# Kernel tuning notes

Measured on AMD Instinct MI355X. Metric: run time of the kernel, lower is better.

Reference implementation:

```python
import jax, jax.numpy as jnp
import numpy as np

N_NODES = 20000
N_EDGES = 320000
N_GRAPHS = 64


def gat_conv(x, src, dst, W, a_src, a_dst, bias, heads, ch, concat):
    # x: [N, F_in]; W: [F_in, heads*ch]; a_src/a_dst: [heads, ch]
    N = x.shape[0]
    h = (x @ W).reshape(N, heads, ch)                       # [N, H, C]
    alpha_s = jnp.sum(h * a_src, axis=-1)                   # [N, H]
    alpha_d = jnp.sum(h * a_dst, axis=-1)                   # [N, H]
    e = jax.nn.leaky_relu(alpha_s[src] + alpha_d[dst], 0.2) # [E, H]
    # segment softmax over incoming edges of each destination node
    m = jax.ops.segment_max(e, dst, num_segments=N)         # [N, H]
    ex = jnp.exp(e - m[dst])
    denom = jax.ops.segment_sum(ex, dst, num_segments=N)    # [N, H]
    alpha = ex / (denom[dst] + 1e-16)                       # [E, H]
    msg = h[src] * alpha[:, :, None]                        # [E, H, C]
    out = jax.ops.segment_sum(msg, dst, num_segments=N)     # [N, H, C]
    out = out.reshape(N, heads * ch) if concat else out.mean(axis=1)
    return out + bias, alpha


def setup_inputs() -> dict:
    key = jax.random.key(0)
    ks = jax.random.split(key, 24)
    dim_in, md, dim_out = 8, 64, 128
    hid = md * 4  # 256
    p = lambda k, shape: jax.random.normal(k, shape, dtype=jnp.float32) * 0.1
    inp = {
        "x_ppi": jax.random.normal(ks[0], (N_NODES, dim_in), dtype=jnp.float32),
        "ppi_edge_index": jax.random.randint(ks[1], (2, N_EDGES), 0, N_NODES),
        "ppi_batch": jnp.sort(jax.random.randint(ks[2], (N_NODES,), 0, N_GRAPHS)),
        # GATConv 1: dim_in -> 64, heads=4, concat
        "W1": p(ks[3], (dim_in, 4 * md)), "a_src1": p(ks[4], (4, md)), "a_dst1": p(ks[5], (4, md)), "b_gat1": jnp.zeros((hid,), jnp.float32),
        "lw1": p(ks[6], (dim_in, hid)), "lb1": jnp.zeros((hid,), jnp.float32),
        # GATConv 2: 256 -> 64, heads=4, concat
        "W2": p(ks[7], (hid, 4 * md)), "a_src2": p(ks[8], (4, md)), "a_dst2": p(ks[9], (4, md)), "b_gat2": jnp.zeros((hid,), jnp.float32),
        "lw2": p(ks[10], (hid, hid)), "lb2": jnp.zeros((hid,), jnp.float32),
        # GATConv 3: 256 -> 128, heads=6, concat=False (mean)
        "W3": p(ks[11], (hid, 6 * dim_out)), "a_src3": p(ks[12], (6, dim_out)), "a_dst3": p(ks[13], (6, dim_out)), "b_gat3": jnp.zeros((dim_out,), jnp.float32),
        "lw3": p(ks[14], (hid, dim_out)), "lb3": jnp.zeros((dim_out,), jnp.float32),
        # BatchNorm1d(dim_out), training-mode batch statistics
        "bn_gamma": jnp.ones((dim_out,), jnp.float32), "bn_beta": jnp.zeros((dim_out,), jnp.float32),
    }
    return inp


def reference(x_ppi, ppi_edge_index, ppi_batch,
              W1, a_src1, a_dst1, b_gat1, lw1, lb1,
              W2, a_src2, a_dst2, b_gat2, lw2, lb2,
              W3, a_src3, a_dst3, b_gat3, lw3, lb3,
              bn_gamma, bn_beta):
    src, dst = ppi_edge_index[0], ppi_edge_index[1]
    g1, _ = gat_conv(x_ppi, src, dst, W1, a_src1, a_dst1, b_gat1, heads=4, ch=64, concat=True)
    x = jax.nn.relu(g1 + x_ppi @ lw1 + lb1)
    g2, _ = gat_conv(x, src, dst, W2, a_src2, a_dst2, b_gat2, heads=4, ch=64, concat=True)
    x = jax.nn.relu(g2 + x @ lw2 + lb2)
    x_res = x @ lw3 + lb3
    g3, att = gat_conv(x, src, dst, W3, a_src3, a_dst3, b_gat3, heads=6, ch=128, concat=False)
    x = g3 + x_res
    x = jax.nn.relu(x)
    # BatchNorm1d, training mode (biased variance, eps=1e-5)
    mu = x.mean(axis=0)
    var = jnp.mean((x - mu) ** 2, axis=0)
    x = (x - mu) * jax.lax.rsqrt(var + 1e-5) * bn_gamma + bn_beta
    # global max pool over graphs
    pooled = jax.ops.segment_max(x, ppi_batch, num_segments=N_GRAPHS)
    return pooled, att
```

## Files before the change

kernel.cpp:

```cpp
#include <hip/hip_runtime.h>
#include <hip/hip_bf16.h>
#include <math.h>

#define N_NODES 20000
#define N_EDGES 320000
#define N_GRAPHS 64

typedef __bf16 bf16_t;
typedef bf16_t bf16x8 __attribute__((ext_vector_type(8)));
typedef bf16_t bf16x4 __attribute__((ext_vector_type(4)));
typedef bf16_t bf16x2 __attribute__((ext_vector_type(2)));
typedef float f32x4 __attribute__((ext_vector_type(4)));
typedef float f32x2 __attribute__((ext_vector_type(2)));

__global__ void hist_k(const int* __restrict__ dst, int* __restrict__ deg, int E) {
    int e = blockIdx.x * 256 + threadIdx.x;
    if (e < E) atomicAdd(&deg[dst[e]], 1);
}

__global__ __launch_bounds__(1024) void scan_k(const int* __restrict__ deg,
                                               int* __restrict__ offs,
                                               int* __restrict__ cursor, int n) {
    __shared__ int s_ws[16];
    int tid = threadIdx.x;
    int lane = tid & 63, w = tid >> 6;
    int carry = 0;
    for (int base = 0; base < n; base += 1024) {
        int i = base + tid;
        int v = (i < n) ? deg[i] : 0;
        int x = v;
        #pragma unroll
        for (int off = 1; off < 64; off <<= 1) {
            int t = __shfl_up(x, off);
            if (lane >= off) x += t;
        }
        if (lane == 63) s_ws[w] = x;
        __syncthreads();
        if (tid < 16) {
            int y = s_ws[tid];
            #pragma unroll
            for (int off = 1; off < 16; off <<= 1) {
                int t = __shfl_up(y, off);
                if (tid >= off) y += t;
            }
            s_ws[tid] = y;
        }
        __syncthreads();
        int wbase = (w > 0) ? s_ws[w - 1] : 0;
        int ex = carry + wbase + x - v;
        if (i < n) { offs[i] = ex; cursor[i] = ex; }
        carry += s_ws[15];
        __syncthreads();
    }
    if (tid == 0) offs[n] = carry;
}

__global__ void scatter_k(const int* __restrict__ src, const int* __restrict__ dst,
                          int* __restrict__ cursor, int* __restrict__ csr_src,
                          int* __restrict__ csr_eid, int E) {
    int e = blockIdx.x * 256 + threadIdx.x;
    if (e < E) {
        int d = dst[e];
        int p = atomicAdd(&cursor[d], 1);
        csr_src[p] = src[e];
        csr_eid[p] = e;
    }
}

__global__ __launch_bounds__(256) void wt_k(const float* __restrict__ W,
                                            bf16_t* __restrict__ Bt, int K, int N) {
    __shared__ float t[32][33];
    int k0 = blockIdx.y * 32, n0 = blockIdx.x * 32;
    int tx = threadIdx.x & 31, ty = threadIdx.x >> 5;
    for (int i = ty; i < 32; i += 8) t[i][tx] = W[(size_t)(k0 + i) * N + n0 + tx];
    __syncthreads();
    for (int i = ty; i < 32; i += 8)
        Bt[(size_t)(n0 + i) * K + k0 + tx] = (bf16_t)t[tx][i];
}

template <typename OUT>
__global__ __launch_bounds__(256) void gemm_k(const float* __restrict__ A,
                                              const float* __restrict__ B,
                                              OUT* __restrict__ C,
                                              const float* __restrict__ bias,
                                              int M, int N, int K,
                                              const float* __restrict__ asv,
                                              const float* __restrict__ adv,
                                              float* __restrict__ as_o,
                                              float* __restrict__ ad_o,
                                              int H, int Ch) {
    __shared__ float As[16][65];
    __shared__ float Bs[16][64];
    int tid = threadIdx.x;
    int tx = tid & 15, ty = tid >> 4;
    int row0 = blockIdx.y * 64, col0 = blockIdx.x * 64;
    float acc[4][4] = {};
    for (int k0 = 0; k0 < K; k0 += 16) {
        #pragma unroll
        for (int i = 0; i < 4; ++i) {
            int idx = tid + i * 256;
            int m = idx >> 4, kk = idx & 15;
            int gm = row0 + m, gk = k0 + kk;
            As[kk][m] = (gm < M && gk < K) ? A[(size_t)gm * K + gk] : 0.f;
        }
        #pragma unroll
        for (int i = 0; i < 4; ++i) {
            int idx = tid + i * 256;
            int kk = idx >> 6, n = idx & 63;
            int gk = k0 + kk, gn = col0 + n;
            Bs[kk][n] = (gk < K && gn < N) ? B[(size_t)gk * N + gn] : 0.f;
        }
        __syncthreads();
        #pragma unroll
        for (int kk = 0; kk < 16; ++kk) {
            float a[4], b[4];
            #pragma unroll
            for (int i = 0; i < 4; ++i) a[i] = As[kk][ty * 4 + i];
            #pragma unroll
            for (int j = 0; j < 4; ++j) b[j] = Bs[kk][tx * 4 + j];
            #pragma unroll
            for (int i = 0; i < 4; ++i)
                #pragma unroll
                for (int j = 0; j < 4; ++j) acc[i][j] += a[i] * b[j];
        }
        __syncthreads();
    }
    #pragma unroll
    for (int i = 0; i < 4; ++i) {
        int gm = row0 + ty * 4 + i;
        if (gm >= M) continue;
        #pragma unroll
        for (int j = 0; j < 4; ++j) {
            int gn = col0 + tx * 4 + j;
            if (gn < N) C[(size_t)gm * N + gn] = (OUT)(acc[i][j] + (bias ? bias[gn] : 0.f));
        }
    }
    if (asv) {
        int hd = col0 / Ch;
        float av[4], dv[4];
        #pragma unroll
        for (int j = 0; j < 4; ++j) {
            int ca = col0 + tx * 4 + j;
            av[j] = asv[ca];
            dv[j] = adv[ca];
        }
        #pragma unroll
        for (int i = 0; i < 4; ++i) {
            float sp = 0.f, sd = 0.f;
            #pragma unroll
            for (int j = 0; j < 4; ++j) { sp += acc[i][j] * av[j]; sd += acc[i][j] * dv[j]; }
            #pragma unroll
            for (int m = 1; m < 16; m <<= 1) {
                sp += __shfl_xor(sp, m);
                sd += __shfl_xor(sd, m);
            }
            if (tx == 0) {
                int gm = row0 + ty * 4 + i;
                if (gm < M) { as_o[gm * H + hd] = sp; ad_o[gm * H + hd] = sd; }
            }
        }
    }
}

template <typename OUT>
__global__ __launch_bounds__(256) void gemm_bf16_k(
    const bf16_t* __restrict__ A, const bf16_t* __restrict__ Bt,
    OUT* __restrict__ C, const float* __restrict__ bias, int M, int N, int K,
    const float* __restrict__ asv, const float* __restrict__ adv,
    float* __restrict__ as_o, float* __restrict__ ad_o, int H, int Ch) {
    __shared__ bf16_t As[128][40];
    __shared__ bf16_t Bs[128][40];
    int tid = threadIdx.x;
    int row0 = blockIdx.y * 128, col0 = blockIdx.x * 128;
    int wave = tid >> 6, lane = tid & 63, quad = lane >> 4, l16 = lane & 15;
    int wm = wave >> 1, wn = wave & 1;
    f32x4 acc[4][4] = {};
    int sr = tid >> 2;
    int sc = (tid & 3) * 8;
    for (int k0 = 0; k0 < K; k0 += 32) {
        #pragma unroll
        for (int half = 0; half < 2; ++half) {
            int r = sr + half * 64;
            int gm = row0 + r;
            bf16x8 v = {};
            if (gm < M) v = *(const bf16x8*)&A[(size_t)gm * K + k0 + sc];
            *(bf16x8*)&As[r][sc] = v;
            int gn = col0 + r;
            bf16x8 w = {};
            if (gn < N) w = *(const bf16x8*)&Bt[(size_t)gn * K + k0 + sc];
            *(bf16x8*)&Bs[r][sc] = w;
        }
        __syncthreads();
        bf16x8 af[4], bfr[4];
        #pragma unroll
        for (int i = 0; i < 4; ++i) {
            af[i] = *(const bf16x8*)&As[wm * 64 + i * 16 + l16][quad * 8];
            bfr[i] = *(const bf16x8*)&Bs[wn * 64 + i * 16 + l16][quad * 8];
        }
        #pragma unroll
        for (int i = 0; i < 4; ++i)
            #pragma unroll
            for (int j = 0; j < 4; ++j)
                acc[i][j] = __builtin_amdgcn_mfma_f32_16x16x32_bf16(af[i], bfr[j],
                                                                   acc[i][j], 0, 0, 0);
        __syncthreads();
    }
    #pragma unroll
    for (int i = 0; i < 4; ++i) {
        int base_m = row0 + wm * 64 + i * 16 + quad * 4;
        #pragma unroll
        for (int j = 0; j < 4; ++j) {
            int gn = col0 + wn * 64 + j * 16 + l16;
            float bv = bias ? bias[gn] : 0.f;
            #pragma unroll
            for (int r = 0; r < 4; ++r) {
                int gm = base_m + r;
                if (gm < M) C[(size_t)gm * N + gn] = (OUT)(acc[i][j][r] + bv);
            }
        }
    }
    if (asv) {
        int hd = (col0 + wn * 64) / Ch;
        float av[4], dv[4];
        #pragma unroll
        for (int j = 0; j < 4; ++j) {
            int ca = col0 + wn * 64 + j * 16 + l16;
            av[j] = asv[ca];
            dv[j] = adv[ca];
        }
        #pragma unroll
        for (int i = 0; i < 4; ++i) {
            float sp[4] = {}, sd[4] = {};
            #pragma unroll
            for (int j = 0; j < 4; ++j)
                #pragma unroll
                for (int r = 0; r < 4; ++r) {
                    sp[r] += acc[i][j][r] * av[j];
                    sd[r] += acc[i][j][r] * dv[j];
                }
            #pragma unroll
            for (int m = 1; m < 16; m <<= 1)
                #pragma unroll
                for (int r = 0; r < 4; ++r) {
                    sp[r] += __shfl_xor(sp[r], m);
                    sd[r] += __shfl_xor(sd[r], m);
                }
            if (l16 == 0) {
                #pragma unroll
                for (int r = 0; r < 4; ++r) {
                    int gm = row0 + wm * 64 + i * 16 + quad * 4 + r;
                    if (gm < M) {
                        if (Ch == 128) {
                            atomicAdd(&as_o[gm * H + hd], sp[r]);
                            atomicAdd(&ad_o[gm * H + hd], sd[r]);
                        } else {
                            as_o[gm * H + hd] = sp[r];
                            ad_o[gm * H + hd] = sd[r];
                        }
                    }
                }
            }
        }
    }
}

__device__ __forceinline__ float leaky02(float v) { return v > 0.f ? v : 0.2f * v; }

__global__ __launch_bounds__(256) void agg_concat_k(
    const bf16_t* __restrict__ h, const float* __restrict__ as_,
    const float* __restrict__ ad_, const int* __restrict__ offs,
    const int* __restrict__ csr_src, const float* __restrict__ lin,
    const float* __restrict__ bgat, bf16_t* __restrict__ xb) {
    int j = blockIdx.x;
    int tid = threadIdx.x;
    int o0 = offs[j], deg = offs[j + 1] - o0;
    __shared__ int s_src[64];
    __shared__ float s_adj[4];
    __shared__ float s_ws[8][4];
    __shared__ float s_inv[4];
    __shared__ float s_red[8][256];
    if (tid < 4) s_adj[tid] = ad_[j * 4 + tid];
    int g = tid >> 5;
    int u = tid & 31;
    int myh = u >> 3;
    const char* hbase = (const char*)h + u * 16;
    f32x4 acc0 = {}, acc1 = {};
    float wsum = 0.f;
    for (int e0 = 0; e0 < deg; e0 += 64) {
        int ne = min(64, deg - e0);
        if (tid < ne) s_src[tid] = csr_src[o0 + e0 + tid];
        __syncthreads();
        float adj = s_adj[myh];
        #pragma unroll 2
        for (int e = g; e < ne; e += 8) {
            int s = s_src[e];
            float w = __expf(leaky02(as_[s * 4 + myh] + adj));
            bf16x8 v = *(const bf16x8*)(hbase + s * 512);
            wsum += w;
            #pragma unroll
            for (int i = 0; i < 4; ++i) acc0[i] += w * (float)v[i];
            #pragma unroll
            for (int i = 0; i < 4; ++i) acc1[i] += w * (float)v[4 + i];
        }
        __syncthreads();
    }
    if ((u & 7) == 0) s_ws[g][myh] = wsum;
    *(f32x4*)&s_red[g][u * 8] = acc0;
    *(f32x4*)&s_red[g][u * 8 + 4] = acc1;
    __syncthreads();
    if (tid < 4) {
        float d = 0.f;
        #pragma unroll
        for (int g2 = 0; g2 < 8; ++g2) d += s_ws[g2][tid];
        s_inv[tid] = 1.f / (d + 1e-16f);
    }
    __syncthreads();
    {
        int c = tid;
        float s = 0.f;
        #pragma unroll
        for (int g2 = 0; g2 < 8; ++g2) s += s_red[g2][c];
        float v = fmaxf(s * s_inv[c >> 6] + bgat[c] + lin[(size_t)j * 256 + c], 0.f);
        xb[(size_t)j * 256 + c] = (bf16_t)v;
    }
}

__global__ __launch_bounds__(256) void agg_mean_k(
    const bf16_t* __restrict__ h, const float* __restrict__ as_,
    const float* __restrict__ ad_, const int* __restrict__ offs,
    const int* __restrict__ csr_src, const int* __restrict__ csr_eid,
    const float* __restrict__ xres, const float* __restrict__ bgat,
    float* __restrict__ y, float* __restrict__ att) {
    int j = blockIdx.x;
    int tid = threadIdx.x;
    int o0 = offs[j], deg = offs[j + 1] - o0;
    __shared__ int s_src[64];
    __shared__ float s_adj[6];
    __shared__ float s_ws[2][6];
    __shared__ float s_inv[6];
    __shared__ float s_red[2][768];
    if (tid < 6) s_adj[tid] = ad_[j * 6 + tid];
    int g = tid / 96;
    int u = tid - g * 96;
    int myh = u >> 4;
    const char* hbase = (const char*)h + u * 16;
    f32x4 acc0 = {}, acc1 = {};
    float wsum = 0.f;
    for (int e0 = 0; e0 < deg; e0 += 64) {
        int ne = min(64, deg - e0);
        if (tid < ne) s_src[tid] = csr_src[o0 + e0 + tid];
        __syncthreads();
        if (tid < 192) {
            float adj = s_adj[myh];
            #pragma unroll 4
            for (int e = g; e < ne; e += 2) {
                int s = s_src[e];
                float w = __expf(leaky02(as_[s * 6 + myh] + adj));
                bf16x8 v = *(const bf16x8*)(hbase + s * 1536);
                wsum += w;
                #pragma unroll
                for (int i = 0; i < 4; ++i) acc0[i] += w * (float)v[i];
                #pragma unroll
                for (int i = 0; i < 4; ++i) acc1[i] += w * (float)v[4 + i];
            }
        }
        __syncthreads();
    }
    if (tid < 192) {
        if ((u & 15) == 0) s_ws[g][myh] = wsum;
        *(f32x4*)&s_red[g][u * 8] = acc0;
        *(f32x4*)&s_red[g][u * 8 + 4] = acc1;
    }
    __syncthreads();
    if (tid < 6) {
        float d = s_ws[0][tid] + s_ws[1][tid];
        s_inv[tid] = 1.f / (d + 1e-16f);
    }
    __syncthreads();
    if (tid < 128) {
        float s = 0.f;
        #pragma unroll
        for (int hh = 0; hh < 6; ++hh)
            s += (s_red[0][hh * 128 + tid] + s_red[1][hh * 128 + tid]) * s_inv[hh];
        y[(size_t)j * 128 + tid] =
            fmaxf(s * (1.f / 6.f) + bgat[tid] + xres[(size_t)j * 128 + tid], 0.f);
    } else if (tid >= 192) {
        int t = tid - 192;
        for (int e = t; e < deg; e += 64) {
            int p = o0 + e;
            int s = csr_src[p];
            size_t eid = (size_t)csr_eid[p];
            #pragma unroll
            for (int hh = 0; hh < 6; ++hh) {
                float w = __expf(leaky02(as_[s * 6 + hh] + s_adj[hh])) * s_inv[hh];
                att[eid * 6 + hh] = w;
            }
        }
    }
}

__global__ void bn_stats_k(const float* __restrict__ y, float* __restrict__ sums, int N) {
    int c = threadIdx.x;
    float s = 0.f, q = 0.f;
    for (int r = blockIdx.x; r < N; r += gridDim.x) {
        float v = y[(size_t)r * 128 + c];
        s += v;
        q += v * v;
    }
    atomicAdd(&sums[c], s);
    atomicAdd(&sums[128 + c], q);
}
__global__ void bn_scale_k(const float* __restrict__ sums, const float* __restrict__ gamma,
                           const float* __restrict__ beta, float* __restrict__ scale,
                           float* __restrict__ shift, int N) {
    int c = threadIdx.x;
    float mu = sums[c] / (float)N;
    float var = fmaxf(sums[128 + c] / (float)N - mu * mu, 0.f);
    float inv = rsqrtf(var + 1e-5f) * gamma[c];
    scale[c] = inv;
    shift[c] = beta[c] - mu * inv;
}

__device__ __forceinline__ unsigned f2key(float f) {
    unsigned b = __float_as_uint(f);
    return (b & 0x80000000u) ? ~b : (b | 0x80000000u);
}
__global__ void pool_init_k(unsigned* __restrict__ pool_u) {
    int i = blockIdx.x * 256 + threadIdx.x;
    if (i < N_GRAPHS * 128) pool_u[i] = f2key(-3.402823466e38f * 2.0f);
}
__global__ void norm_pool_k(const float* __restrict__ y, const float* __restrict__ scale,
                            const float* __restrict__ shift, const int* __restrict__ batch,
                            unsigned* __restrict__ pool_u, int N) {
    int idx = blockIdx.x * 256 + threadIdx.x;
    if (idx >= N * 128) return;
    int n = idx >> 7, c = idx & 127;
    float v = y[idx] * scale[c] + shift[c];
    atomicMax(&pool_u[batch[n] * 128 + c], f2key(v));
}
__global__ void pool_write_k(const unsigned* __restrict__ pool_u, float* __restrict__ out) {
    int i = blockIdx.x * 256 + threadIdx.x;
    if (i < N_GRAPHS * 128) {
        unsigned u = pool_u[i];
        unsigned b = (u & 0x80000000u) ? (u & 0x7FFFFFFFu) : ~u;
        out[i] = __uint_as_float(b);
    }
}

extern "C" void kernel_launch(void* const* d_in, const int* in_sizes, int n_in,
                              void* d_out, int out_size, void* d_ws, size_t ws_size,
                              hipStream_t stream) {
    const int N = N_NODES, E = N_EDGES;
    const float* x_ppi = (const float*)d_in[0];
    const int* edge = (const int*)d_in[1];
    const int* batch = (const int*)d_in[2];
    const float* W1 = (const float*)d_in[3];
    const float* a_src1 = (const float*)d_in[4];
    const float* a_dst1 = (const float*)d_in[5];
    const float* b_gat1 = (const float*)d_in[6];
    const float* lw1 = (const float*)d_in[7];
    const float* lb1 = (const float*)d_in[8];
    const float* W2 = (const float*)d_in[9];
    const float* a_src2 = (const float*)d_in[10];
    const float* a_dst2 = (const float*)d_in[11];
    const float* b_gat2 = (const float*)d_in[12];
    const float* lw2 = (const float*)d_in[13];
    const float* lb2 = (const float*)d_in[14];
    const float* W3 = (const float*)d_in[15];
    const float* a_src3 = (const float*)d_in[16];
    const float* a_dst3 = (const float*)d_in[17];
    const float* b_gat3 = (const float*)d_in[18];
    const float* lw3 = (const float*)d_in[19];
    const float* lb3 = (const float*)d_in[20];
    const float* bn_gamma = (const float*)d_in[21];
    const float* bn_beta = (const float*)d_in[22];

    const int* src = edge;
    const int* dst = edge + E;

    size_t off = 0;
    auto alloc = [&](size_t bytes) {
        size_t o = off;
        off = (off + bytes + 255) & ~(size_t)255;
        return o;
    };
    char* ws = (char*)d_ws;
    bf16_t* xb = (bf16_t*)(ws + alloc((size_t)N * 256 * 2));
    bf16_t* hb = (bf16_t*)(ws + alloc((size_t)N * 768 * 2));
    float* lin = (float*)(ws + alloc((size_t)N * 256 * 4));
    float* x_res = (float*)(ws + alloc((size_t)N * 128 * 4));
    float* as_ = (float*)(ws + alloc((size_t)N * 6 * 4));
    float* ad_ = (float*)(ws + alloc((size_t)N * 6 * 4));
    int* deg = (int*)(ws + alloc((size_t)(N + 1) * 4));
    int* offs = (int*)(ws + alloc((size_t)(N + 1) * 4));
    int* cursor = (int*)(ws + alloc((size_t)(N + 1) * 4));
    int* csr_src = (int*)(ws + alloc((size_t)E * 4));
    int* csr_eid = (int*)(ws + alloc((size_t)E * 4));
    bf16_t* Wt2 = (bf16_t*)(ws + alloc((size_t)256 * 256 * 2));
    bf16_t* lwt2 = (bf16_t*)(ws + alloc((size_t)256 * 256 * 2));
    bf16_t* Wt3 = (bf16_t*)(ws + alloc((size_t)768 * 256 * 2));
    bf16_t* lwt3 = (bf16_t*)(ws + alloc((size_t)128 * 256 * 2));
    float* bn_sums = (float*)(ws + alloc(256 * 4));
    float* bn_scale = (float*)(ws + alloc(128 * 4));
    float* bn_shift = (float*)(ws + alloc(128 * 4));
    unsigned* pool_u = (unsigned*)(ws + alloc((size_t)N_GRAPHS * 128 * 4));

    float* out_pool = (float*)d_out;
    float* out_att = (float*)d_out + N_GRAPHS * 128;

    hipMemsetAsync(deg, 0, (size_t)N * 4, stream);
    hist_k<<<(E + 255) / 256, 256, 0, stream>>>(dst, deg, E);
    scan_k<<<1, 1024, 0, stream>>>(deg, offs, cursor, N);
    scatter_k<<<(E + 255) / 256, 256, 0, stream>>>(src, dst, cursor, csr_src, csr_eid, E);
    wt_k<<<dim3(8, 8), 256, 0, stream>>>(W2, Wt2, 256, 256);
    wt_k<<<dim3(8, 8), 256, 0, stream>>>(lw2, lwt2, 256, 256);
    wt_k<<<dim3(24, 8), 256, 0, stream>>>(W3, Wt3, 256, 768);
    wt_k<<<dim3(4, 8), 256, 0, stream>>>(lw3, lwt3, 256, 128);

    gemm_k<bf16_t><<<dim3(4, 313), 256, 0, stream>>>(x_ppi, W1, hb, nullptr, N, 256, 8,
                                                     a_src1, a_dst1, as_, ad_, 4, 64);
    gemm_k<float><<<dim3(4, 313), 256, 0, stream>>>(x_ppi, lw1, lin, lb1, N, 256, 8,
                                                    nullptr, nullptr, nullptr, nullptr, 0, 1);
    agg_concat_k<<<N, 256, 0, stream>>>(hb, as_, ad_, offs, csr_src, lin, b_gat1, xb);

    gemm_bf16_k<bf16_t><<<dim3(2, 157), 256, 0, stream>>>(xb, Wt2, hb, nullptr, N, 256, 256,
                                                          a_src2, a_dst2, as_, ad_, 4, 64);
    gemm_bf16_k<float><<<dim3(2, 157), 256, 0, stream>>>(xb, lwt2, lin, lb2, N, 256, 256,
                                                         nullptr, nullptr, nullptr, nullptr,
                                                         0, 1);
    agg_concat_k<<<N, 256, 0, stream>>>(hb, as_, ad_, offs, csr_src, lin, b_gat2, xb);

    hipMemsetAsync(as_, 0, (size_t)N * 6 * 4, stream);
    hipMemsetAsync(ad_, 0, (size_t)N * 6 * 4, stream);
    gemm_bf16_k<bf16_t><<<dim3(6, 157), 256, 0, stream>>>(xb, Wt3, hb, nullptr, N, 768, 256,
                                                          a_src3, a_dst3, as_, ad_, 6, 128);
    gemm_bf16_k<float><<<dim3(1, 157), 256, 0, stream>>>(xb, lwt3, x_res, lb3, N, 128, 256,
                                                         nullptr, nullptr, nullptr, nullptr,
                                                         0, 1);
    float* y = lin;
    agg_mean_k<<<N, 256, 0, stream>>>(hb, as_, ad_, offs, csr_src, csr_eid, x_res, b_gat3,
                                      y, out_att);

    hipMemsetAsync(bn_sums, 0, 256 * 4, stream);
    bn_stats_k<<<160, 128, 0, stream>>>(y, bn_sums, N);
    bn_scale_k<<<1, 128, 0, stream>>>(bn_sums, bn_gamma, bn_beta, bn_scale, bn_shift, N);

    pool_init_k<<<(N_GRAPHS * 128 + 255) / 256, 256, 0, stream>>>(pool_u);
    norm_pool_k<<<((size_t)N * 128 + 255) / 256, 256, 0, stream>>>(y, bn_scale, bn_shift, batch,
                                                                   pool_u, N);
    pool_write_k<<<(N_GRAPHS * 128 + 255) / 256, 256, 0, stream>>>(pool_u, out_pool);
}
```

Measured before the change: 525.6 us.

## Aggregate before projecting in GAT layers 1 and 3 using linearity

Layers 1 and 3 now aggregate the input features before the projection instead of projecting then aggregating. The attention logits come from precomputed W·a vectors, and the mean over heads, the residual linear and the biases are folded into one stacked GEMM (K=40 for layer 1, K=1792 for layer 3). This removes the large 768-wide hidden tensor and its per-edge gathers in layer 3, which now gather 256-wide rows. In exchange layer 3 writes a 1792-wide per-node buffer and runs a longer-K GEMM, and bf16 rounding moves to different points in the computation.

```diff
diff --git a/kernel.cpp b/kernel.cpp
--- a/kernel.cpp
+++ b/kernel.cpp
@@ -78,17 +78,69 @@
         Bt[(size_t)(n0 + i) * K + k0 + tx] = (bf16_t)t[tx][i];
 }
 
+__global__ void w3s_k(const float* __restrict__ W3, const float* __restrict__ lw3,
+                      bf16_t* __restrict__ Bt) {
+    int id = blockIdx.x * 256 + threadIdx.x;
+    if (id >= 128 * 1792) return;
+    int n = id / 1792, k = id - n * 1792;
+    float v;
+    if (k < 1536) {
+        int h = k >> 8, c = k & 255;
+        v = W3[(size_t)c * 768 + h * 128 + n] * (1.f / 6.f);
+    } else {
+        int c = k - 1536;
+        v = lw3[(size_t)c * 128 + n];
+    }
+    Bt[id] = (bf16_t)v;
+}
+
+__global__ void b40_k(const float* __restrict__ W1, const float* __restrict__ lw1,
+                      float* __restrict__ B) {
+    int id = blockIdx.x * 256 + threadIdx.x;
+    if (id >= 40 * 256) return;
+    int k = id >> 8, n = id & 255;
+    float v;
+    if (k < 32) {
+        int h = k >> 3, c = k & 7;
+        v = ((n >> 6) == h) ? W1[(size_t)c * 256 + n] : 0.f;
+    } else {
+        int c = k - 32;
+        v = lw1[(size_t)c * 256 + n];
+    }
+    B[id] = v;
+}
+
+__global__ void va_k(const float* __restrict__ W, const float* __restrict__ a_s,
+                     const float* __restrict__ a_d, float* __restrict__ Va,
+                     float* __restrict__ Vd, int H, int C) {
+    int k = blockIdx.x;
+    int lane = threadIdx.x;
+    const float* wr = W + (size_t)k * H * C;
+    for (int h = 0; h < H; ++h) {
+        float sa = 0.f, sd = 0.f;
+        for (int c = lane; c < C; c += 64) {
+            float wv = wr[h * C + c];
+            sa += wv * a_s[h * C + c];
+            sd += wv * a_d[h * C + c];
+        }
+        #pragma unroll
+        for (int m = 32; m; m >>= 1) { sa += __shfl_xor(sa, m); sd += __shfl_xor(sd, m); }
+        if (lane == 0) { Va[k * H + h] = sa; Vd[k * H + h] = sd; }
+    }
+}
+
+__global__ void addb_k(const float* __restrict__ a, const float* __restrict__ b,
+                       float* __restrict__ o, int n) {
+    int i = blockIdx.x * 256 + threadIdx.x;
+    if (i < n) o[i] = a[i] + b[i];
+}
+
 template <typename OUT>
 __global__ __launch_bounds__(256) void gemm_k(const float* __restrict__ A,
                                               const float* __restrict__ B,
                                               OUT* __restrict__ C,
                                               const float* __restrict__ bias,
-                                              int M, int N, int K,
-                                              const float* __restrict__ asv,
-                                              const float* __restrict__ adv,
-                                              float* __restrict__ as_o,
-                                              float* __restrict__ ad_o,
-                                              int H, int Ch) {
+                                              int M, int N, int K, int relu) {
     __shared__ float As[16][65];
     __shared__ float Bs[16][64];
     int tid = threadIdx.x;
@@ -132,31 +184,10 @@
         #pragma unroll
         for (int j = 0; j < 4; ++j) {
             int gn = col0 + tx * 4 + j;
-            if (gn < N) C[(size_t)gm * N + gn] = (OUT)(acc[i][j] + (bias ? bias[gn] : 0.f));
-        }
-    }
-    if (asv) {
-        int hd = col0 / Ch;
-        float av[4], dv[4];
-        #pragma unroll
-        for (int j = 0; j < 4; ++j) {
-            int ca = col0 + tx * 4 + j;
-            av[j] = asv[ca];
-            dv[j] = adv[ca];
-        }
-        #pragma unroll
-        for (int i = 0; i < 4; ++i) {
-            float sp = 0.f, sd = 0.f;
-            #pragma unroll
-            for (int j = 0; j < 4; ++j) { sp += acc[i][j] * av[j]; sd += acc[i][j] * dv[j]; }
-            #pragma unroll
-            for (int m = 1; m < 16; m <<= 1) {
-                sp += __shfl_xor(sp, m);
-                sd += __shfl_xor(sd, m);
-            }
-            if (tx == 0) {
-                int gm = row0 + ty * 4 + i;
-                if (gm < M) { as_o[gm * H + hd] = sp; ad_o[gm * H + hd] = sd; }
+            if (gn < N) {
+                float r = acc[i][j] + (bias ? bias[gn] : 0.f);
+                if (relu) r = fmaxf(r, 0.f);
+                C[(size_t)gm * N + gn] = (OUT)r;
             }
         }
     }
@@ -167,7 +198,7 @@
     const bf16_t* __restrict__ A, const bf16_t* __restrict__ Bt,
     OUT* __restrict__ C, const float* __restrict__ bias, int M, int N, int K,
     const float* __restrict__ asv, const float* __restrict__ adv,
-    float* __restrict__ as_o, float* __restrict__ ad_o, int H, int Ch) {
+    float* __restrict__ as_o, float* __restrict__ ad_o, int H, int Ch, int relu) {
     __shared__ bf16_t As[128][40];
     __shared__ bf16_t Bs[128][40];
     int tid = threadIdx.x;
@@ -215,7 +246,11 @@
             #pragma unroll
             for (int r = 0; r < 4; ++r) {
                 int gm = base_m + r;
-                if (gm < M) C[(size_t)gm * N + gn] = (OUT)(acc[i][j][r] + bv);
+                if (gm < M) {
+                    float rr = acc[i][j][r] + bv;
+                    if (relu) rr = fmaxf(rr, 0.f);
+                    C[(size_t)gm * N + gn] = (OUT)rr;
+                }
             }
         }
     }
@@ -250,13 +285,8 @@
                 for (int r = 0; r < 4; ++r) {
                     int gm = row0 + wm * 64 + i * 16 + quad * 4 + r;
                     if (gm < M) {
-                        if (Ch == 128) {
-                            atomicAdd(&as_o[gm * H + hd], sp[r]);
-                            atomicAdd(&ad_o[gm * H + hd], sd[r]);
-                        } else {
-                            as_o[gm * H + hd] = sp[r];
-                            ad_o[gm * H + hd] = sd[r];
-                        }
+                        as_o[gm * H + hd] = sp[r];
+                        ad_o[gm * H + hd] = sd[r];
                     }
                 }
             }
@@ -265,6 +295,90 @@
 }
 
 __device__ __forceinline__ float leaky02(float v) { return v > 0.f ? v : 0.2f * v; }
+
+__global__ void asad1_k(const float* __restrict__ x, const float* __restrict__ Va,
+                        const float* __restrict__ Vd, float* __restrict__ as_,
+                        float* __restrict__ ad_, int N) {
+    int idx = blockIdx.x * 256 + threadIdx.x;
+    if (idx >= N * 4) return;
+    int j = idx >> 2, h = idx & 3;
+    const float* xr = x + (size_t)j * 8;
+    float sa = 0.f, sd = 0.f;
+    #pragma unroll
+    for (int c = 0; c < 8; ++c) {
+        sa += xr[c] * Va[c * 4 + h];
+        sd += xr[c] * Vd[c * 4 + h];
+    }
+    as_[idx] = sa;
+    ad_[idx] = sd;
+}
+
+__global__ void asad3_k(const bf16_t* __restrict__ xb, const float* __restrict__ Va,
+                        const float* __restrict__ Vd, float* __restrict__ as_,
+                        float* __restrict__ ad_) {
+    int j = blockIdx.x;
+    int lane = threadIdx.x;
+    bf16x4 v = *(const bf16x4*)&xb[(size_t)j * 256 + lane * 4];
+    float sa[6] = {}, sd[6] = {};
+    #pragma unroll
+    for (int i = 0; i < 4; ++i) {
+        int k = lane * 4 + i;
+        float xv = (float)v[i];
+        #pragma unroll
+        for (int h = 0; h < 6; ++h) {
+            sa[h] += xv * Va[k * 6 + h];
+            sd[h] += xv * Vd[k * 6 + h];
+        }
+    }
+    #pragma unroll
+    for (int h = 0; h < 6; ++h) {
+        float a = sa[h], d = sd[h];
+        #pragma unroll
+        for (int m = 32; m; m >>= 1) { a += __shfl_xor(a, m); d += __shfl_xor(d, m); }
+        if (lane == 0) { as_[j * 6 + h] = a; ad_[j * 6 + h] = d; }
+    }
+}
+
+__global__ __launch_bounds__(256) void agg_z1_k(
+    const float* __restrict__ x, const float* __restrict__ as_,
+    const float* __restrict__ ad_, const int* __restrict__ offs,
+    const int* __restrict__ csr_src, float* __restrict__ z1) {
+    int j = blockIdx.x * 4 + (threadIdx.x >> 6);
+    int t = threadIdx.x & 63;
+    int e_l = t >> 3, c = t & 7;
+    int o0 = offs[j], deg = offs[j + 1] - o0;
+    float adj0 = ad_[j * 4 + 0], adj1 = ad_[j * 4 + 1];
+    float adj2 = ad_[j * 4 + 2], adj3 = ad_[j * 4 + 3];
+    float acc[4] = {}, ws[4] = {};
+    for (int e0 = 0; e0 < deg; e0 += 8) {
+        int ne = min(8, deg - e0);
+        if (e_l < ne) {
+            int s = csr_src[o0 + e0 + e_l];
+            float xv = x[(size_t)s * 8 + c];
+            f32x4 a = *(const f32x4*)&as_[s * 4];
+            float w0 = __expf(leaky02(a[0] + adj0));
+            float w1 = __expf(leaky02(a[1] + adj1));
+            float w2 = __expf(leaky02(a[2] + adj2));
+            float w3 = __expf(leaky02(a[3] + adj3));
+            acc[0] += w0 * xv; acc[1] += w1 * xv;
+            acc[2] += w2 * xv; acc[3] += w3 * xv;
+            ws[0] += w0; ws[1] += w1; ws[2] += w2; ws[3] += w3;
+        }
+    }
+    #pragma unroll
+    for (int m = 8; m < 64; m <<= 1)
+        #pragma unroll
+        for (int h = 0; h < 4; ++h) {
+            acc[h] += __shfl_xor(acc[h], m);
+            ws[h] += __shfl_xor(ws[h], m);
+        }
+    if (e_l == 0) {
+        #pragma unroll
+        for (int h = 0; h < 4; ++h)
+            z1[(size_t)j * 40 + h * 8 + c] = acc[h] / (ws[h] + 1e-16f);
+        z1[(size_t)j * 40 + 32 + c] = x[(size_t)j * 8 + c];
+    }
+}
 
 __global__ __launch_bounds__(256) void agg_concat_k(
     const bf16_t* __restrict__ h, const float* __restrict__ as_,
@@ -295,7 +409,7 @@
         for (int e = g; e < ne; e += 8) {
             int s = s_src[e];
             float w = __expf(leaky02(as_[s * 4 + myh] + adj));
-            bf16x8 v = *(const bf16x8*)(hbase + s * 512);
+            bf16x8 v = *(const bf16x8*)(hbase + (size_t)s * 512);
             wsum += w;
             #pragma unroll
             for (int i = 0; i < 4; ++i) acc0[i] += w * (float)v[i];
@@ -325,77 +439,86 @@
     }
 }
 
-__global__ __launch_bounds__(256) void agg_mean_k(
-    const bf16_t* __restrict__ h, const float* __restrict__ as_,
+__global__ __launch_bounds__(256) void agg_z3_k(
+    const bf16_t* __restrict__ xb, const float* __restrict__ as_,
     const float* __restrict__ ad_, const int* __restrict__ offs,
     const int* __restrict__ csr_src, const int* __restrict__ csr_eid,
-    const float* __restrict__ xres, const float* __restrict__ bgat,
-    float* __restrict__ y, float* __restrict__ att) {
+    bf16_t* __restrict__ z, float* __restrict__ att) {
     int j = blockIdx.x;
     int tid = threadIdx.x;
     int o0 = offs[j], deg = offs[j + 1] - o0;
+    __shared__ float s_adj[6], s_denom[6], s_inv[6];
     __shared__ int s_src[64];
-    __shared__ float s_adj[6];
-    __shared__ float s_ws[2][6];
-    __shared__ float s_inv[6];
-    __shared__ float s_red[2][768];
-    if (tid < 6) s_adj[tid] = ad_[j * 6 + tid];
-    int g = tid / 96;
-    int u = tid - g * 96;
-    int myh = u >> 4;
-    const char* hbase = (const char*)h + u * 16;
-    f32x4 acc0 = {}, acc1 = {};
-    float wsum = 0.f;
+    __shared__ float s_w[64 * 6];
+    __shared__ float s_red[8][6][256];
+    if (tid < 6) { s_adj[tid] = ad_[j * 6 + tid]; s_denom[tid] = 0.f; }
+    __syncthreads();
+    int g = tid >> 5;
+    int c = tid & 31;
+    const char* xbase = (const char*)xb + c * 16;
+    f32x4 a0[6] = {}, a1[6] = {};
     for (int e0 = 0; e0 < deg; e0 += 64) {
         int ne = min(64, deg - e0);
-        if (tid < ne) s_src[tid] = csr_src[o0 + e0 + tid];
-        __syncthreads();
-        if (tid < 192) {
-            float adj = s_adj[myh];
-            #pragma unroll 4
-            for (int e = g; e < ne; e += 2) {
-                int s = s_src[e];
-                float w = __expf(leaky02(as_[s * 6 + myh] + adj));
-                bf16x8 v = *(const bf16x8*)(hbase + s * 1536);
-                wsum += w;
+        #pragma unroll
+        for (int base = 0; base < 2; ++base) {
+            int idx = tid + base * 256;
+            if (idx < ne * 6) {
+                int e = idx / 6, h = idx - e * 6;
+                int s = csr_src[o0 + e0 + e];
+                if (h == 0) s_src[e] = s;
+                s_w[idx] = __expf(leaky02(as_[s * 6 + h] + s_adj[h]));
+            }
+        }
+        __syncthreads();
+        if (tid < 6) {
+            float d = 0.f;
+            for (int e = 0; e < ne; ++e) d += s_w[e * 6 + tid];
+            s_denom[tid] += d;
+        }
+        for (int e = g; e < ne; e += 8) {
+            int s = s_src[e];
+            bf16x8 v = *(const bf16x8*)(xbase + (size_t)s * 512);
+            float f0[4], f1[4];
+            #pragma unroll
+            for (int i = 0; i < 4; ++i) { f0[i] = (float)v[i]; f1[i] = (float)v[4 + i]; }
+            #pragma unroll
+            for (int h = 0; h < 6; ++h) {
+                float w = s_w[e * 6 + h];
                 #pragma unroll
-                for (int i = 0; i < 4; ++i) acc0[i] += w * (float)v[i];
-                #pragma unroll
-                for (int i = 0; i < 4; ++i) acc1[i] += w * (float)v[4 + i];
+                for (int i = 0; i < 4; ++i) {
+                    a0[h][i] += w * f0[i];
+                    a1[h][i] += w * f1[i];
+                }
             }
         }
         __syncthreads();
     }
-    if (tid < 192) {
-        if ((u & 15) == 0) s_ws[g][myh] = wsum;
-        *(f32x4*)&s_red[g][u * 8] = acc0;
-        *(f32x4*)&s_red[g][u * 8 + 4] = acc1;
-    }
+    #pragma unroll
+    for (int h = 0; h < 6; ++h) {
+        *(f32x4*)&s_red[g][h][c * 8] = a0[h];
+        *(f32x4*)&s_red[g][h][c * 8 + 4] = a1[h];
+    }
+    if (tid < 6) s_inv[tid] = 1.f / (s_denom[tid] + 1e-16f);
     __syncthreads();
-    if (tid < 6) {
-        float d = s_ws[0][tid] + s_ws[1][tid];
-        s_inv[tid] = 1.f / (d + 1e-16f);
-    }
-    __syncthreads();
-    if (tid < 128) {
-        float s = 0.f;
-        #pragma unroll
-        for (int hh = 0; hh < 6; ++hh)
-            s += (s_red[0][hh * 128 + tid] + s_red[1][hh * 128 + tid]) * s_inv[hh];
-        y[(size_t)j * 128 + tid] =
-            fmaxf(s * (1.f / 6.f) + bgat[tid] + xres[(size_t)j * 128 + tid], 0.f);
-    } else if (tid >= 192) {
-        int t = tid - 192;
-        for (int e = t; e < deg; e += 64) {
-            int p = o0 + e;
-            int s = csr_src[p];
-            size_t eid = (size_t)csr_eid[p];
-            #pragma unroll
-            for (int hh = 0; hh < 6; ++hh) {
-                float w = __expf(leaky02(as_[s * 6 + hh] + s_adj[hh])) * s_inv[hh];
-                att[eid * 6 + hh] = w;
-            }
-        }
+    {
+        int cc = tid;
+        #pragma unroll
+        for (int h = 0; h < 6; ++h) {
+            float s = 0.f;
+            #pragma unroll
+            for (int g2 = 0; g2 < 8; ++g2) s += s_red[g2][h][cc];
+            z[(size_t)j * 1792 + h * 256 + cc] = (bf16_t)(s * s_inv[h]);
+        }
+    }
+    if (tid < 32)
+        *(bf16x8*)&z[(size_t)j * 1792 + 1536 + tid * 8] =
+            *(const bf16x8*)&xb[(size_t)j * 256 + tid * 8];
+    for (int idx = tid; idx < deg * 6; idx += 256) {
+        int e = idx / 6, h = idx - e * 6;
+        int p = o0 + e;
+        int s = csr_src[p];
+        att[(size_t)csr_eid[p] * 6 + h] =
+            __expf(leaky02(as_[s * 6 + h] + s_adj[h])) * s_inv[h];
     }
 }
 
@@ -486,9 +609,11 @@
     };
     char* ws = (char*)d_ws;
     bf16_t* xb = (bf16_t*)(ws + alloc((size_t)N * 256 * 2));
-    bf16_t* hb = (bf16_t*)(ws + alloc((size_t)N * 768 * 2));
+    bf16_t* zbig = (bf16_t*)(ws + alloc((size_t)N * 1792 * 2));
+    bf16_t* hb = zbig;
+    bf16_t* z3 = zbig;
     float* lin = (float*)(ws + alloc((size_t)N * 256 * 4));
-    float* x_res = (float*)(ws + alloc((size_t)N * 128 * 4));
+    float* z1 = (float*)(ws + alloc((size_t)N * 40 * 4));
     float* as_ = (float*)(ws + alloc((size_t)N * 6 * 4));
     float* ad_ = (float*)(ws + alloc((size_t)N * 6 * 4));
     int* deg = (int*)(ws + alloc((size_t)(N + 1) * 4));
@@ -498,8 +623,14 @@
     int* csr_eid = (int*)(ws + alloc((size_t)E * 4));
     bf16_t* Wt2 = (bf16_t*)(ws + alloc((size_t)256 * 256 * 2));
     bf16_t* lwt2 = (bf16_t*)(ws + alloc((size_t)256 * 256 * 2));
-    bf16_t* Wt3 = (bf16_t*)(ws + alloc((size_t)768 * 256 * 2));
-    bf16_t* lwt3 = (bf16_t*)(ws + alloc((size_t)128 * 256 * 2));
+    bf16_t* Bt3s = (bf16_t*)(ws + alloc((size_t)128 * 1792 * 2));
+    float* B40 = (float*)(ws + alloc((size_t)40 * 256 * 4));
+    float* Va1 = (float*)(ws + alloc(8 * 4 * 4));
+    float* Vd1 = (float*)(ws + alloc(8 * 4 * 4));
+    float* Va3 = (float*)(ws + alloc(256 * 6 * 4));
+    float* Vd3 = (float*)(ws + alloc(256 * 6 * 4));
+    float* bias1s = (float*)(ws + alloc(256 * 4));
+    float* bias3s = (float*)(ws + alloc(128 * 4));
     float* bn_sums = (float*)(ws + alloc(256 * 4));
     float* bn_scale = (float*)(ws + alloc(128 * 4));
     float* bn_shift = (float*)(ws + alloc(128 * 4));
@@ -514,32 +645,30 @@
     scatter_k<<<(E + 255) / 256, 256, 0, stream>>>(src, dst, cursor, csr_src, csr_eid, E);
     wt_k<<<dim3(8, 8), 256, 0, stream>>>(W2, Wt2, 256, 256);
     wt_k<<<dim3(8, 8), 256, 0, stream>>>(lw2, lwt2, 256, 256);
-    wt_k<<<dim3(24, 8), 256, 0, stream>>>(W3, Wt3, 256, 768);
-    wt_k<<<dim3(4, 8), 256, 0, stream>>>(lw3, lwt3, 256, 128);
-
-    gemm_k<bf16_t><<<dim3(4, 313), 256, 0, stream>>>(x_ppi, W1, hb, nullptr, N, 256, 8,
-                                                     a_src1, a_dst1, as_, ad_, 4, 64);
-    gemm_k<float><<<dim3(4, 313), 256, 0, stream>>>(x_ppi, lw1, lin, lb1, N, 256, 8,
-                                                    nullptr, nullptr, nullptr, nullptr, 0, 1);
-    agg_concat_k<<<N, 256, 0, stream>>>(hb, as_, ad_, offs, csr_src, lin, b_gat1, xb);
+    w3s_k<<<896, 256, 0, stream>>>(W3, lw3, Bt3s);
+    b40_k<<<40, 256, 0, stream>>>(W1, lw1, B40);
+    va_k<<<8, 64, 0, stream>>>(W1, a_src1, a_dst1, Va1, Vd1, 4, 64);
+    va_k<<<256, 64, 0, stream>>>(W3, a_src3, a_dst3, Va3, Vd3, 6, 128);
+    addb_k<<<1, 256, 0, stream>>>(lb1, b_gat1, bias1s, 256);
+    addb_k<<<1, 128, 0, stream>>>(lb3, b_gat3, bias3s, 128);
+
+    asad1_k<<<(N * 4 + 255) / 256, 256, 0, stream>>>(x_ppi, Va1, Vd1, as_, ad_, N);
+    agg_z1_k<<<N / 4, 256, 0, stream>>>(x_ppi, as_, ad_, offs, csr_src, z1);
+    gemm_k<bf16_t><<<dim3(4, 313), 256, 0, stream>>>(z1, B40, xb, bias1s, N, 256, 40, 1);
 
     gemm_bf16_k<bf16_t><<<dim3(2, 157), 256, 0, stream>>>(xb, Wt2, hb, nullptr, N, 256, 256,
-                                                          a_src2, a_dst2, as_, ad_, 4, 64);
+                                                          a_src2, a_dst2, as_, ad_, 4, 64, 0);
     gemm_bf16_k<float><<<dim3(2, 157), 256, 0, stream>>>(xb, lwt2, lin, lb2, N, 256, 256,
                                                          nullptr, nullptr, nullptr, nullptr,
-                                                         0, 1);
+                                                         0, 1, 0);
     agg_concat_k<<<N, 256, 0, stream>>>(hb, as_, ad_, offs, csr_src, lin, b_gat2, xb);
 
-    hipMemsetAsync(as_, 0, (size_t)N * 6 * 4, stream);
-    hipMemsetAsync(ad_, 0, (size_t)N * 6 * 4, stream);
-    gemm_bf16_k<bf16_t><<<dim3(6, 157), 256, 0, stream>>>(xb, Wt3, hb, nullptr, N, 768, 256,
-                                                          a_src3, a_dst3, as_, ad_, 6, 128);
-    gemm_bf16_k<float><<<dim3(1, 157), 256, 0, stream>>>(xb, lwt3, x_res, lb3, N, 128, 256,
+    asad3_k<<<N, 64, 0, stream>>>(xb, Va3, Vd3, as_, ad_);
+    agg_z3_k<<<N, 256, 0, stream>>>(xb, as_, ad_, offs, csr_src, csr_eid, z3, out_att);
+    float* y = lin;
+    gemm_bf16_k<float><<<dim3(1, 157), 256, 0, stream>>>(z3, Bt3s, y, bias3s, N, 128, 1792,
                                                          nullptr, nullptr, nullptr, nullptr,
-                                                         0, 1);
-    float* y = lin;
-    agg_mean_k<<<N, 256, 0, stream>>>(hb, as_, ad_, offs, csr_src, csr_eid, x_res, b_gat3,
-                                      y, out_att);
+                                                         0, 1, 1);
 
     hipMemsetAsync(bn_sums, 0, 256 * 4, stream);
     bn_stats_k<<<160, 128, 0, stream>>>(y, bn_sums, N);
```

Result: slower. 567.0 us (+7.9%).
